# Performance work log

Measured on AMD Instinct MI355X. Metric: run time of the kernel, lower is better.

Reference implementation:

```python
import jax, jax.numpy as jnp
import numpy as np

B, N_LATENT, N_NUISANCE, N_OUT = 2048, 64, 16, 2048


def setup_inputs() -> dict:
    key = jax.random.key(0)
    ks = jax.random.split(key, 6)
    z = jax.random.normal(ks[0], (B, N_LATENT + N_NUISANCE), dtype=jnp.float32)
    size_factor = jax.random.uniform(ks[1], (B, 1), dtype=jnp.float32) + 0.5
    # nn.Linear(n_latent, n_out, bias=False): store as [L, O] for z0 @ W
    amat_w = jax.random.normal(ks[2], (N_LATENT, N_OUT), dtype=jnp.float32) / np.sqrt(N_LATENT).astype(np.float32)
    amat_site = jax.random.normal(ks[3], (N_NUISANCE, N_LATENT, N_OUT), dtype=jnp.float32)
    offsets = jax.random.normal(ks[4], (N_NUISANCE, N_OUT), dtype=jnp.float32)
    px_r = jax.random.normal(ks[5], (N_OUT,), dtype=jnp.float32)
    return {"z": z, "size_factor": size_factor, "amat_w": amat_w,
            "amat_site": amat_site, "offsets": offsets, "px_r": px_r}


def reference(z, size_factor, amat_w, amat_site, offsets, px_r):
    n_nuisance = offsets.shape[0]
    nuisance_oh = z[..., -n_nuisance:]          # [B, N] one-hot site indicator
    z0 = z[..., :-n_nuisance]                   # [B, L] latent part
    x1 = z0 @ amat_w                            # [B, O] shared linear decoder
    nuisance_ids = jnp.argmax(nuisance_oh, axis=-1)  # [B] int ids
    # dropout(p=0.1) in eval mode == identity; .detach() -> stop_gradient
    z0_d = jax.lax.stop_gradient(z0)
    As = amat_site[nuisance_ids]                # [B, L, O] per-sample gathered weights
    x2 = jnp.einsum('bl,blo->bo', z0_d, As)     # batched matvec reduction over L
    mu = jax.nn.softmax(x1 + x2 + offsets[nuisance_ids], axis=-1)  # [B, O]
    mu = mu * size_factor                       # scale by per-cell size factor
    theta = jnp.exp(px_r)                       # NB inverse-dispersion, [O]
    return mu, theta
```

## Files before the change

### kernel.cpp

```cpp
#include <hip/hip_runtime.h>
#include <hip/hip_bf16.h>

#define NB 2048
#define NL 64
#define NN 16
#define NROW 80
#define NO 2048
#define RPB 8
#define MAXG (NB / RPB + NN)
#define CTILE 512
#define NCT (NO / CTILE)

typedef unsigned int   u32;
typedef unsigned short u16;

struct Group { int id; int start; int nr; int pad; };

__device__ __forceinline__ float bflo(u32 u) { union { u32 i; float f; } c; c.i = u << 16;         return c.f; }
__device__ __forceinline__ float bfhi(u32 u) { union { u32 i; float f; } c; c.i = u & 0xffff0000u; return c.f; }
__device__ __forceinline__ u16 f2bf(float f) { __hip_bfloat16 h = __float2bfloat16(f); return *(u16*)&h; }

__global__ __launch_bounds__(1024) void bucket_all(
    const float* __restrict__ z, const float* __restrict__ pxr,
    int* __restrict__ perm, Group* __restrict__ groups, int* __restrict__ ngroups,
    float* __restrict__ out)
{
    __shared__ int cnt[NN], start_s[NN], cur[NN], gbase[NN];
    const int tid = threadIdx.x;
    if (tid < NN) cnt[tid] = 0;
    for (int o = tid; o < NO; o += 1024)
        out[(size_t)NB * NO + o] = __expf(pxr[o]);
    __syncthreads();

    int myid[NB / 1024];
    #pragma unroll
    for (int k = 0; k < NB / 1024; ++k) {
        const int row = tid + k * 1024;
        const float* p = z + (size_t)row * NROW + NL;
        float best = p[0]; int bi = 0;
        #pragma unroll
        for (int i = 1; i < NN; ++i) { float v = p[i]; if (v > best) { best = v; bi = i; } }
        myid[k] = bi;
        atomicAdd(&cnt[bi], 1);
    }
    __syncthreads();
    if (tid == 0) {
        int acc = 0, g = 0;
        for (int i = 0; i < NN; ++i) {
            start_s[i] = acc; cur[i] = acc; gbase[i] = g;
            acc += cnt[i]; g += (cnt[i] + RPB - 1) / RPB;
        }
        *ngroups = g;
    }
    __syncthreads();
    #pragma unroll
    for (int k = 0; k < NB / 1024; ++k) {
        const int row = tid + k * 1024;
        const int pos = atomicAdd(&cur[myid[k]], 1);
        perm[pos] = row;
    }
    if (tid < NN) {
        const int c = cnt[tid], s = start_s[tid], gb = gbase[tid];
        for (int j = 0; j * RPB < c; ++j) {
            Group gr; gr.id = tid; gr.start = s + j * RPB;
            gr.nr = min(RPB, c - j * RPB); gr.pad = 0;
            groups[gb + j] = gr;
        }
    }
}

__global__ __launch_bounds__(256) void build_m(const float* __restrict__ W,
                                               const float* __restrict__ A,
                                               u16* __restrict__ M) {
    size_t t    = (size_t)blockIdx.x * 256 + threadIdx.x;
    size_t base = t * 4;
    float4 w = *(const float4*)(W + (base & (size_t)(NL * NO - 1)));
    float4 a = *(const float4*)(A + base);
    ushort4 m;
    m.x = f2bf(w.x + a.x); m.y = f2bf(w.y + a.y);
    m.z = f2bf(w.z + a.z); m.w = f2bf(w.w + a.w);
    *(ushort4*)(M + base) = m;
}

__global__ __launch_bounds__(256) void gemm_logits(
    const float* __restrict__ z, const u16* __restrict__ M,
    const float* __restrict__ offs, const int* __restrict__ perm,
    const Group* __restrict__ groups, const int* __restrict__ ngroups,
    float* __restrict__ logits)
{
    const int g  = blockIdx.x >> 2;
    const int ct = blockIdx.x & 3;
    if (g >= *ngroups) return;
    const int id     = groups[g].id;
    const int pstart = groups[g].start;
    const int nr     = groups[g].nr;
    const int tid    = threadIdx.x;

    __shared__ int   rows_s[RPB];
    __shared__ float zT[NL][RPB];

    if (tid < RPB) rows_s[tid] = perm[pstart + (tid < nr ? tid : nr - 1)];
    __syncthreads();
    {
        int r = tid >> 6, l = tid & 63;
        zT[l][r] = z[(size_t)rows_s[r] * NROW + l];
        int idx2 = tid + 256; r = idx2 >> 6; l = idx2 & 63;
        zT[l][r] = z[(size_t)rows_s[r] * NROW + l];
    }
    __syncthreads();

    const int c0 = ct * CTILE + tid * 2;
    const u16* Mg = M + (size_t)id * NL * NO + c0;

    float2 acc[RPB];
    {
        float2 o2 = *(const float2*)(offs + id * NO + c0);
        #pragma unroll
        for (int r = 0; r < RPB; ++r) acc[r] = o2;
    }

    #pragma unroll 8
    for (int l = 0; l < NL; ++l) {
        u32 m = *(const u32*)(Mg + (size_t)l * NO);
        float ml = bflo(m), mh = bfhi(m);
        float4 za = *(const float4*)&zT[l][0];
        float4 zb = *(const float4*)&zT[l][4];
        acc[0].x += za.x * ml; acc[0].y += za.x * mh;
        acc[1].x += za.y * ml; acc[1].y += za.y * mh;
        acc[2].x += za.z * ml; acc[2].y += za.z * mh;
        acc[3].x += za.w * ml; acc[3].y += za.w * mh;
        acc[4].x += zb.x * ml; acc[4].y += zb.x * mh;
        acc[5].x += zb.y * ml; acc[5].y += zb.y * mh;
        acc[6].x += zb.z * ml; acc[6].y += zb.z * mh;
        acc[7].x += zb.w * ml; acc[7].y += zb.w * mh;
    }

    for (int r = 0; r < nr; ++r)
        *(float2*)(logits + (size_t)rows_s[r] * NO + c0) = acc[r];
}

__global__ __launch_bounds__(256) void softmax_scale(
    const float* __restrict__ logits, const float* __restrict__ sf,
    float* __restrict__ out)
{
    const int b = blockIdx.x, tid = threadIdx.x, o0 = tid * 8;
    __shared__ float s_red[6];

    const float* lp = logits + (size_t)b * NO + o0;
    float4 v0 = *(const float4*)lp, v1 = *(const float4*)(lp + 4);
    float v[8] = { v0.x, v0.y, v0.z, v0.w, v1.x, v1.y, v1.z, v1.w };

    float m = v[0];
    #pragma unroll
    for (int j = 1; j < 8; ++j) m = fmaxf(m, v[j]);
    #pragma unroll
    for (int off = 32; off > 0; off >>= 1) m = fmaxf(m, __shfl_down(m, off));
    if ((tid & 63) == 0) s_red[tid >> 6] = m;
    __syncthreads();
    if (tid == 0) s_red[4] = fmaxf(fmaxf(s_red[0], s_red[1]), fmaxf(s_red[2], s_red[3]));
    __syncthreads();
    const float mx = s_red[4];

    float s = 0.f;
    #pragma unroll
    for (int j = 0; j < 8; ++j) { v[j] = __expf(v[j] - mx); s += v[j]; }
    #pragma unroll
    for (int off = 32; off > 0; off >>= 1) s += __shfl_down(s, off);
    if ((tid & 63) == 0) s_red[tid >> 6] = s;
    __syncthreads();
    if (tid == 0) s_red[5] = (s_red[0] + s_red[1]) + (s_red[2] + s_red[3]);
    __syncthreads();
    const float scl = sf[b] / s_red[5];

    float* op = out + (size_t)b * NO + o0;
    *(float4*)(op)     = make_float4(v[0] * scl, v[1] * scl, v[2] * scl, v[3] * scl);
    *(float4*)(op + 4) = make_float4(v[4] * scl, v[5] * scl, v[6] * scl, v[7] * scl);
}

__global__ __launch_bounds__(256) void decoder_f(
    const float* __restrict__ z, const float* __restrict__ sf,
    const float* __restrict__ W, const float* __restrict__ A,
    const float* __restrict__ offs, const float* __restrict__ pxr,
    float* __restrict__ out)
{
    const int b   = blockIdx.x;
    const int tid = threadIdx.x;
    if (b == NB) {
        for (int o = tid; o < NO; o += 256) out[(size_t)NB * NO + o] = __expf(pxr[o]);
        return;
    }
    __shared__ float z0s[NL];
    __shared__ int   s_id;
    __shared__ float s_red[6];
    if (tid < NL) z0s[tid] = z[b * NROW + tid];
    if (tid == 0) {
        float best = -1e30f; int bi = 0;
        for (int i = 0; i < NN; ++i) { float v = z[b * NROW + NL + i]; if (v > best) { best = v; bi = i; } }
        s_id = bi;
    }
    __syncthreads();
    const int id = s_id;
    const int o0 = tid * 8;
    const float* wp = W + o0;
    const float* ap = A + (size_t)id * NL * NO + o0;
    float acc[8];
    {
        float4 oa = *(const float4*)(offs + id * NO + o0);
        float4 ob = *(const float4*)(offs + id * NO + o0 + 4);
        acc[0]=oa.x; acc[1]=oa.y; acc[2]=oa.z; acc[3]=oa.w;
        acc[4]=ob.x; acc[5]=ob.y; acc[6]=ob.z; acc[7]=ob.w;
    }
    #pragma unroll 4
    for (int l = 0; l < NL; ++l) {
        const float zl = z0s[l];
        float4 w0 = *(const float4*)(wp + l * NO);
        float4 w1 = *(const float4*)(wp + l * NO + 4);
        float4 a0 = *(const float4*)(ap + l * NO);
        float4 a1 = *(const float4*)(ap + l * NO + 4);
        acc[0] += zl * (w0.x + a0.x); acc[1] += zl * (w0.y + a0.y);
        acc[2] += zl * (w0.z + a0.z); acc[3] += zl * (w0.w + a0.w);
        acc[4] += zl * (w1.x + a1.x); acc[5] += zl * (w1.y + a1.y);
        acc[6] += zl * (w1.z + a1.z); acc[7] += zl * (w1.w + a1.w);
    }
    float m = acc[0];
    #pragma unroll
    for (int j = 1; j < 8; ++j) m = fmaxf(m, acc[j]);
    #pragma unroll
    for (int off = 32; off > 0; off >>= 1) m = fmaxf(m, __shfl_down(m, off));
    if ((tid & 63) == 0) s_red[tid >> 6] = m;
    __syncthreads();
    if (tid == 0) s_red[4] = fmaxf(fmaxf(s_red[0], s_red[1]), fmaxf(s_red[2], s_red[3]));
    __syncthreads();
    const float mx = s_red[4];
    float ex[8];
    float s = 0.f;
    #pragma unroll
    for (int j = 0; j < 8; ++j) { ex[j] = __expf(acc[j] - mx); s += ex[j]; }
    #pragma unroll
    for (int off = 32; off > 0; off >>= 1) s += __shfl_down(s, off);
    if ((tid & 63) == 0) s_red[tid >> 6] = s;
    __syncthreads();
    if (tid == 0) s_red[5] = (s_red[0] + s_red[1]) + (s_red[2] + s_red[3]);
    __syncthreads();
    const float scale = sf[b] / s_red[5];
    float* op = out + (size_t)b * NO + o0;
    *(float4*)(op)     = make_float4(ex[0]*scale, ex[1]*scale, ex[2]*scale, ex[3]*scale);
    *(float4*)(op + 4) = make_float4(ex[4]*scale, ex[5]*scale, ex[6]*scale, ex[7]*scale);
}

extern "C" void kernel_launch(void* const* d_in, const int* in_sizes, int n_in,
                              void* d_out, int out_size, void* d_ws, size_t ws_size,
                              hipStream_t stream) {
    const float* z    = (const float*)d_in[0];
    const float* sf   = (const float*)d_in[1];
    const float* W    = (const float*)d_in[2];
    const float* A    = (const float*)d_in[3];
    const float* offs = (const float*)d_in[4];
    const float* pxr  = (const float*)d_in[5];
    float* out = (float*)d_out;

    const size_t M_OFF = 0, PERM_OFF = 4u << 20, GRP_OFF = (4u << 20) + 8192,
                 NG_OFF = (4u << 20) + 16384, LG_OFF = 8u << 20;
    const size_t ws_need = LG_OFF + (size_t)NB * NO * sizeof(float);
    if (ws_size >= ws_need) {
        char* wsb = (char*)d_ws;
        u16*   M       = (u16*)(wsb + M_OFF);
        int*   perm    = (int*)(wsb + PERM_OFF);
        Group* groups  = (Group*)(wsb + GRP_OFF);
        int*   ngroups = (int*)(wsb + NG_OFF);
        float* logits  = (float*)(wsb + LG_OFF);
        hipLaunchKernelGGL(bucket_all, dim3(1), dim3(1024), 0, stream, z, pxr, perm, groups, ngroups, out);
        hipLaunchKernelGGL(build_m, dim3((NN * NL * NO / 4) / 256), dim3(256), 0, stream, W, A, M);
        hipLaunchKernelGGL(gemm_logits, dim3(MAXG * NCT), dim3(256), 0, stream,
                           z, M, offs, perm, groups, ngroups, logits);
        hipLaunchKernelGGL(softmax_scale, dim3(NB), dim3(256), 0, stream, logits, sf, out);
    } else {
        hipLaunchKernelGGL(decoder_f, dim3(NB + 1), dim3(256), 0, stream, z, sf, W, A, offs, pxr, out);
    }
}
```

Measured before the change: 118.5 us.

## Fuse softmax into grouped GEMM and merge bucketing with weight conversion

Each gemm block now covers all 2048 output columns for its group of up to 8 same-site rows and performs the row softmax and size-factor scaling in place. This removes the 16 MB logits round trip through global memory and the separate softmax launch. The bucketing kernel and the bf16 weight-merge kernel become one launch, with block 0 doing a parallel 4-lanes-per-row argmax. Per-block work grows while block count drops to about 272, which risks under-filling the GPU and raising register pressure from 32 accumulators per thread.

```diff
diff --git a/kernel.cpp b/kernel.cpp
--- a/kernel.cpp
+++ b/kernel.cpp
@@ -8,8 +8,6 @@
 #define NO 2048
 #define RPB 8
 #define MAXG (NB / RPB + NN)
-#define CTILE 512
-#define NCT (NO / CTILE)
 
 typedef unsigned int   u32;
 typedef unsigned short u16;
@@ -20,161 +18,183 @@
 __device__ __forceinline__ float bfhi(u32 u) { union { u32 i; float f; } c; c.i = u & 0xffff0000u; return c.f; }
 __device__ __forceinline__ u16 f2bf(float f) { __hip_bfloat16 h = __float2bfloat16(f); return *(u16*)&h; }
 
-__global__ __launch_bounds__(1024) void bucket_all(
+__global__ __launch_bounds__(512) void prep(
     const float* __restrict__ z, const float* __restrict__ pxr,
-    int* __restrict__ perm, Group* __restrict__ groups, int* __restrict__ ngroups,
-    float* __restrict__ out)
+    const float* __restrict__ W, const float* __restrict__ A,
+    u16* __restrict__ M, int* __restrict__ perm, Group* __restrict__ groups,
+    int* __restrict__ ngroups, float* __restrict__ out)
 {
-    __shared__ int cnt[NN], start_s[NN], cur[NN], gbase[NN];
     const int tid = threadIdx.x;
+
+    if (blockIdx.x != 0) {
+        size_t i = ((size_t)(blockIdx.x - 1) * 512 + tid) * 4;
+        float4 w = *(const float4*)(W + (i & (size_t)(NL * NO - 1)));
+        float4 a = *(const float4*)(A + i);
+        ushort4 m;
+        m.x = f2bf(w.x + a.x); m.y = f2bf(w.y + a.y);
+        m.z = f2bf(w.z + a.z); m.w = f2bf(w.w + a.w);
+        *(ushort4*)(M + i) = m;
+        return;
+    }
+
+    __shared__ int cnt[NN], start_s[NN], cur[NN], gbase_s[NN];
+    __shared__ int ids_sh[NB];
+
     if (tid < NN) cnt[tid] = 0;
-    for (int o = tid; o < NO; o += 1024)
+    for (int o = tid; o < NO; o += 512)
         out[(size_t)NB * NO + o] = __expf(pxr[o]);
     __syncthreads();
 
-    int myid[NB / 1024];
-    #pragma unroll
-    for (int k = 0; k < NB / 1024; ++k) {
-        const int row = tid + k * 1024;
-        const float* p = z + (size_t)row * NROW + NL;
-        float best = p[0]; int bi = 0;
-        #pragma unroll
-        for (int i = 1; i < NN; ++i) { float v = p[i]; if (v > best) { best = v; bi = i; } }
-        myid[k] = bi;
-        atomicAdd(&cnt[bi], 1);
-    }
-    __syncthreads();
+    const int c = tid & 3;
+    #pragma unroll 4
+    for (int pass = 0; pass < 16; ++pass) {
+        const int row = pass * 128 + (tid >> 2);
+        float4 v = *(const float4*)(z + (size_t)row * NROW + NL + c * 4);
+        float bv = v.x; int bp = c * 4;
+        if (v.y > bv) { bv = v.y; bp = c * 4 + 1; }
+        if (v.z > bv) { bv = v.z; bp = c * 4 + 2; }
+        if (v.w > bv) { bv = v.w; bp = c * 4 + 3; }
+        #pragma unroll
+        for (int d = 1; d <= 2; d <<= 1) {
+            float ov = __shfl_xor(bv, d);
+            int   op = __shfl_xor(bp, d);
+            if (ov > bv || (ov == bv && op < bp)) { bv = ov; bp = op; }
+        }
+        if (c == 0) { ids_sh[row] = bp; atomicAdd(&cnt[bp], 1); }
+    }
+    __syncthreads();
+
     if (tid == 0) {
         int acc = 0, g = 0;
         for (int i = 0; i < NN; ++i) {
-            start_s[i] = acc; cur[i] = acc; gbase[i] = g;
+            start_s[i] = acc; cur[i] = acc; gbase_s[i] = g;
             acc += cnt[i]; g += (cnt[i] + RPB - 1) / RPB;
         }
         *ngroups = g;
     }
     __syncthreads();
-    #pragma unroll
-    for (int k = 0; k < NB / 1024; ++k) {
-        const int row = tid + k * 1024;
-        const int pos = atomicAdd(&cur[myid[k]], 1);
+
+    #pragma unroll
+    for (int k = 0; k < NB / 512; ++k) {
+        const int row = tid + k * 512;
+        const int id  = ids_sh[row];
+        const int pos = atomicAdd(&cur[id], 1);
         perm[pos] = row;
     }
     if (tid < NN) {
-        const int c = cnt[tid], s = start_s[tid], gb = gbase[tid];
-        for (int j = 0; j * RPB < c; ++j) {
+        const int cn = cnt[tid], s = start_s[tid], gb = gbase_s[tid];
+        for (int j = 0; j * RPB < cn; ++j) {
             Group gr; gr.id = tid; gr.start = s + j * RPB;
-            gr.nr = min(RPB, c - j * RPB); gr.pad = 0;
+            gr.nr = min(RPB, cn - j * RPB); gr.pad = 0;
             groups[gb + j] = gr;
         }
     }
 }
 
-__global__ __launch_bounds__(256) void build_m(const float* __restrict__ W,
-                                               const float* __restrict__ A,
-                                               u16* __restrict__ M) {
-    size_t t    = (size_t)blockIdx.x * 256 + threadIdx.x;
-    size_t base = t * 4;
-    float4 w = *(const float4*)(W + (base & (size_t)(NL * NO - 1)));
-    float4 a = *(const float4*)(A + base);
-    ushort4 m;
-    m.x = f2bf(w.x + a.x); m.y = f2bf(w.y + a.y);
-    m.z = f2bf(w.z + a.z); m.w = f2bf(w.w + a.w);
-    *(ushort4*)(M + base) = m;
-}
-
-__global__ __launch_bounds__(256) void gemm_logits(
-    const float* __restrict__ z, const u16* __restrict__ M,
-    const float* __restrict__ offs, const int* __restrict__ perm,
-    const Group* __restrict__ groups, const int* __restrict__ ngroups,
-    float* __restrict__ logits)
+__global__ __launch_bounds__(512, 2) void gemm_fused(
+    const float* __restrict__ z, const float* __restrict__ sf,
+    const u16* __restrict__ M, const float* __restrict__ offs,
+    const int* __restrict__ perm, const Group* __restrict__ groups,
+    const int* __restrict__ ngroups, float* __restrict__ out)
 {
-    const int g  = blockIdx.x >> 2;
-    const int ct = blockIdx.x & 3;
+    const int g = blockIdx.x;
     if (g >= *ngroups) return;
     const int id     = groups[g].id;
     const int pstart = groups[g].start;
     const int nr     = groups[g].nr;
     const int tid    = threadIdx.x;
+    const int lane   = tid & 63, wave = tid >> 6;
 
     __shared__ int   rows_s[RPB];
     __shared__ float zT[NL][RPB];
+    __shared__ float sfs[RPB];
+    __shared__ float red[8][RPB];
+    __shared__ float gmax[RPB], gsum[RPB];
 
     if (tid < RPB) rows_s[tid] = perm[pstart + (tid < nr ? tid : nr - 1)];
     __syncthreads();
     {
-        int r = tid >> 6, l = tid & 63;
+        const int r = tid >> 6, l = tid & 63;
         zT[l][r] = z[(size_t)rows_s[r] * NROW + l];
-        int idx2 = tid + 256; r = idx2 >> 6; l = idx2 & 63;
-        zT[l][r] = z[(size_t)rows_s[r] * NROW + l];
-    }
-    __syncthreads();
-
-    const int c0 = ct * CTILE + tid * 2;
+    }
+    if (tid < RPB) sfs[tid] = sf[rows_s[tid]];
+    __syncthreads();
+
+    const int c0 = tid * 4;
     const u16* Mg = M + (size_t)id * NL * NO + c0;
 
-    float2 acc[RPB];
+    float acc[RPB][4];
     {
-        float2 o2 = *(const float2*)(offs + id * NO + c0);
-        #pragma unroll
-        for (int r = 0; r < RPB; ++r) acc[r] = o2;
+        float4 o4 = *(const float4*)(offs + id * NO + c0);
+        #pragma unroll
+        for (int r = 0; r < RPB; ++r) {
+            acc[r][0] = o4.x; acc[r][1] = o4.y; acc[r][2] = o4.z; acc[r][3] = o4.w;
+        }
     }
 
     #pragma unroll 8
     for (int l = 0; l < NL; ++l) {
-        u32 m = *(const u32*)(Mg + (size_t)l * NO);
-        float ml = bflo(m), mh = bfhi(m);
+        uint2 m = *(const uint2*)(Mg + (size_t)l * NO);
+        float m0 = bflo(m.x), m1 = bfhi(m.x), m2 = bflo(m.y), m3 = bfhi(m.y);
         float4 za = *(const float4*)&zT[l][0];
         float4 zb = *(const float4*)&zT[l][4];
-        acc[0].x += za.x * ml; acc[0].y += za.x * mh;
-        acc[1].x += za.y * ml; acc[1].y += za.y * mh;
-        acc[2].x += za.z * ml; acc[2].y += za.z * mh;
-        acc[3].x += za.w * ml; acc[3].y += za.w * mh;
-        acc[4].x += zb.x * ml; acc[4].y += zb.x * mh;
-        acc[5].x += zb.y * ml; acc[5].y += zb.y * mh;
-        acc[6].x += zb.z * ml; acc[6].y += zb.z * mh;
-        acc[7].x += zb.w * ml; acc[7].y += zb.w * mh;
-    }
-
-    for (int r = 0; r < nr; ++r)
-        *(float2*)(logits + (size_t)rows_s[r] * NO + c0) = acc[r];
-}
-
-__global__ __launch_bounds__(256) void softmax_scale(
-    const float* __restrict__ logits, const float* __restrict__ sf,
-    float* __restrict__ out)
-{
-    const int b = blockIdx.x, tid = threadIdx.x, o0 = tid * 8;
-    __shared__ float s_red[6];
-
-    const float* lp = logits + (size_t)b * NO + o0;
-    float4 v0 = *(const float4*)lp, v1 = *(const float4*)(lp + 4);
-    float v[8] = { v0.x, v0.y, v0.z, v0.w, v1.x, v1.y, v1.z, v1.w };
-
-    float m = v[0];
-    #pragma unroll
-    for (int j = 1; j < 8; ++j) m = fmaxf(m, v[j]);
-    #pragma unroll
-    for (int off = 32; off > 0; off >>= 1) m = fmaxf(m, __shfl_down(m, off));
-    if ((tid & 63) == 0) s_red[tid >> 6] = m;
-    __syncthreads();
-    if (tid == 0) s_red[4] = fmaxf(fmaxf(s_red[0], s_red[1]), fmaxf(s_red[2], s_red[3]));
-    __syncthreads();
-    const float mx = s_red[4];
-
-    float s = 0.f;
-    #pragma unroll
-    for (int j = 0; j < 8; ++j) { v[j] = __expf(v[j] - mx); s += v[j]; }
-    #pragma unroll
-    for (int off = 32; off > 0; off >>= 1) s += __shfl_down(s, off);
-    if ((tid & 63) == 0) s_red[tid >> 6] = s;
-    __syncthreads();
-    if (tid == 0) s_red[5] = (s_red[0] + s_red[1]) + (s_red[2] + s_red[3]);
-    __syncthreads();
-    const float scl = sf[b] / s_red[5];
-
-    float* op = out + (size_t)b * NO + o0;
-    *(float4*)(op)     = make_float4(v[0] * scl, v[1] * scl, v[2] * scl, v[3] * scl);
-    *(float4*)(op + 4) = make_float4(v[4] * scl, v[5] * scl, v[6] * scl, v[7] * scl);
+        acc[0][0] += za.x * m0; acc[0][1] += za.x * m1; acc[0][2] += za.x * m2; acc[0][3] += za.x * m3;
+        acc[1][0] += za.y * m0; acc[1][1] += za.y * m1; acc[1][2] += za.y * m2; acc[1][3] += za.y * m3;
+        acc[2][0] += za.z * m0; acc[2][1] += za.z * m1; acc[2][2] += za.z * m2; acc[2][3] += za.z * m3;
+        acc[3][0] += za.w * m0; acc[3][1] += za.w * m1; acc[3][2] += za.w * m2; acc[3][3] += za.w * m3;
+        acc[4][0] += zb.x * m0; acc[4][1] += zb.x * m1; acc[4][2] += zb.x * m2; acc[4][3] += zb.x * m3;
+        acc[5][0] += zb.y * m0; acc[5][1] += zb.y * m1; acc[5][2] += zb.y * m2; acc[5][3] += zb.y * m3;
+        acc[6][0] += zb.z * m0; acc[6][1] += zb.z * m1; acc[6][2] += zb.z * m2; acc[6][3] += zb.z * m3;
+        acc[7][0] += zb.w * m0; acc[7][1] += zb.w * m1; acc[7][2] += zb.w * m2; acc[7][3] += zb.w * m3;
+    }
+
+    float rv[RPB];
+    #pragma unroll
+    for (int r = 0; r < RPB; ++r) {
+        float mv = fmaxf(fmaxf(acc[r][0], acc[r][1]), fmaxf(acc[r][2], acc[r][3]));
+        #pragma unroll
+        for (int off = 32; off > 0; off >>= 1) mv = fmaxf(mv, __shfl_down(mv, off));
+        rv[r] = mv;
+    }
+    if (lane == 0) {
+        for (int r = 0; r < RPB; ++r) red[wave][r] = rv[r];
+    }
+    __syncthreads();
+    if (tid < RPB) {
+        float mm = red[0][tid];
+        #pragma unroll
+        for (int w = 1; w < 8; ++w) mm = fmaxf(mm, red[w][tid]);
+        gmax[tid] = mm;
+    }
+    __syncthreads();
+
+    #pragma unroll
+    for (int r = 0; r < RPB; ++r) {
+        const float mx = gmax[r];
+        float s = 0.f;
+        #pragma unroll
+        for (int cc = 0; cc < 4; ++cc) { acc[r][cc] = __expf(acc[r][cc] - mx); s += acc[r][cc]; }
+        #pragma unroll
+        for (int off = 32; off > 0; off >>= 1) s += __shfl_down(s, off);
+        rv[r] = s;
+    }
+    if (lane == 0) {
+        for (int r = 0; r < RPB; ++r) red[wave][r] = rv[r];
+    }
+    __syncthreads();
+    if (tid < RPB) {
+        float ss = 0.f;
+        #pragma unroll
+        for (int w = 0; w < 8; ++w) ss += red[w][tid];
+        gsum[tid] = ss;
+    }
+    __syncthreads();
+
+    for (int r = 0; r < nr; ++r) {
+        const float scl = sfs[r] / gsum[r];
+        *(float4*)(out + (size_t)rows_s[r] * NO + c0) =
+            make_float4(acc[r][0] * scl, acc[r][1] * scl, acc[r][2] * scl, acc[r][3] * scl);
+    }
 }
 
 __global__ __launch_bounds__(256) void decoder_f(
@@ -260,20 +280,18 @@
     float* out = (float*)d_out;
 
     const size_t M_OFF = 0, PERM_OFF = 4u << 20, GRP_OFF = (4u << 20) + 8192,
-                 NG_OFF = (4u << 20) + 16384, LG_OFF = 8u << 20;
-    const size_t ws_need = LG_OFF + (size_t)NB * NO * sizeof(float);
+                 NG_OFF = (4u << 20) + 16384;
+    const size_t ws_need = NG_OFF + 256;
     if (ws_size >= ws_need) {
         char* wsb = (char*)d_ws;
         u16*   M       = (u16*)(wsb + M_OFF);
         int*   perm    = (int*)(wsb + PERM_OFF);
         Group* groups  = (Group*)(wsb + GRP_OFF);
         int*   ngroups = (int*)(wsb + NG_OFF);
-        float* logits  = (float*)(wsb + LG_OFF);
-        hipLaunchKernelGGL(bucket_all, dim3(1), dim3(1024), 0, stream, z, pxr, perm, groups, ngroups, out);
-        hipLaunchKernelGGL(build_m, dim3((NN * NL * NO / 4) / 256), dim3(256), 0, stream, W, A, M);
-        hipLaunchKernelGGL(gemm_logits, dim3(MAXG * NCT), dim3(256), 0, stream,
-                           z, M, offs, perm, groups, ngroups, logits);
-        hipLaunchKernelGGL(softmax_scale, dim3(NB), dim3(256), 0, stream, logits, sf, out);
+        hipLaunchKernelGGL(prep, dim3(1 + (NN * NL * NO / 4) / 512), dim3(512), 0, stream,
+                           z, pxr, W, A, M, perm, groups, ngroups, out);
+        hipLaunchKernelGGL(gemm_fused, dim3(MAXG), dim3(512), 0, stream,
+                           z, sf, M, offs, perm, groups, ngroups, out);
     } else {
         hipLaunchKernelGGL(decoder_f, dim3(NB + 1), dim3(256), 0, stream, z, sf, W, A, offs, pxr, out);
     }
```

After: 108.8 us. 8.2% less time.
